# Kernel tuning notes

Measured on AMD Instinct MI355X. Metric: run time of the kernel, lower is better.

The kernel has to match this reference:

```python
import jax, jax.numpy as jnp
import numpy as np

EPS = 1e-6


def layernorm(x, g, b):
    m = jnp.mean(x, axis=-1, keepdims=True)
    v = jnp.var(x, axis=-1, keepdims=True)
    return (x - m) * jax.lax.rsqrt(v + EPS) * g + b


def dwconv(x, w, b):
    # x: (B,H,W,C), w: (kh,kw,1,C) depthwise kernel, SAME padding (stride 1)
    y = jax.lax.conv_general_dilated(
        x, w, window_strides=(1, 1), padding='SAME',
        dimension_numbers=('NHWC', 'HWIO', 'NHWC'),
        feature_group_count=x.shape[-1])
    return y + b


def setup_inputs() -> dict:
    key = jax.random.key(0)
    ks = jax.random.split(key, 16)
    B, H, W, C = 16, 64, 64, 256
    N, F = 8, 1024
    s = 0.02
    return {
        'x': jax.random.normal(ks[0], (B, H, W, C), jnp.float32),
        'mask_h': jax.random.normal(ks[1], (N, H, H), jnp.float32),
        'mask_w': jax.random.normal(ks[2], (N, W, W), jnp.float32),
        'pos_w': jax.random.normal(ks[3], (3, 3, 1, C), jnp.float32) * s,
        'pos_b': jnp.zeros((C,), jnp.float32),
        'ln1_g': jnp.ones((C,), jnp.float32),
        'ln1_b': jnp.zeros((C,), jnp.float32),
        'wq': jax.random.normal(ks[4], (C, C), jnp.float32) * s,
        'bq': jnp.zeros((C,), jnp.float32),
        'wk': jax.random.normal(ks[5], (C, C), jnp.float32) * s,
        'bk': jnp.zeros((C,), jnp.float32),
        'wv': jax.random.normal(ks[6], (C, C), jnp.float32) * s,
        'bv': jnp.zeros((C,), jnp.float32),
        'lepe_w': jax.random.normal(ks[7], (5, 5, 1, C), jnp.float32) * s,
        'lepe_b': jnp.zeros((C,), jnp.float32),
        'wo': jax.random.normal(ks[8], (C, C), jnp.float32) * s,
        'bo': jnp.zeros((C,), jnp.float32),
        'ln2_g': jnp.ones((C,), jnp.float32),
        'ln2_b': jnp.zeros((C,), jnp.float32),
        'fc1_w': jax.random.normal(ks[9], (C, F), jnp.float32) * s,
        'fc1_b': jnp.zeros((F,), jnp.float32),
        'fc2_w': jax.random.normal(ks[10], (F, C), jnp.float32) * s,
        'fc2_b': jnp.zeros((C,), jnp.float32),
    }


NUM_HEADS = 8


def masad(x, mask_h, mask_w, wq, bq, wk, bk, wv, bv, lepe_w, lepe_b, wo, bo):
    # x: (B,H,W,C); decomposed axial retention (MaSAd)
    B, H, W, C = x.shape
    n = NUM_HEADS
    d = C // n
    scaling = d ** (-0.5)
    q = x @ wq + bq
    k = (x @ wk + bk) * scaling
    v = x @ wv + bv
    lepe = dwconv(v, lepe_w, lepe_b)  # (B,H,W,C)
    q5 = q.reshape(B, H, W, n, d)
    k5 = k.reshape(B, H, W, n, d)
    v5 = v.reshape(B, H, W, n, d)
    # --- W-axis attention: scores (B,H,n,W,W)
    qk_w = jnp.einsum('bhqnd,bhknd->bhnqk', q5, k5)
    Aw = jax.nn.softmax(qk_w + mask_w[None, None], axis=-1)
    vo = jnp.einsum('bhnqk,bhknd->bhqnd', Aw, v5)  # (B,H,W,n,d)
    # --- H-axis attention: scores (B,W,n,H,H)
    qk_h = jnp.einsum('bqwnd,bkwnd->bwnqk', q5, k5)
    Ah = jax.nn.softmax(qk_h + mask_h[None, None], axis=-1)
    out = jnp.einsum('bwnqk,bkwnd->bqwnd', Ah, vo)  # (B,H,W,n,d)
    out = out.reshape(B, H, W, C) + lepe
    return out @ wo + bo


def reference(x, mask_h, mask_w, pos_w, pos_b, ln1_g, ln1_b,
              wq, bq, wk, bk, wv, bv, lepe_w, lepe_b, wo, bo,
              ln2_g, ln2_b, fc1_w, fc1_b, fc2_w, fc2_b):
    x = x + dwconv(x, pos_w, pos_b)
    x = x + masad(layernorm(x, ln1_g, ln1_b), mask_h, mask_w,
                  wq, bq, wk, bk, wv, bv, lepe_w, lepe_b, wo, bo)
    h = layernorm(x, ln2_g, ln2_b)
    h = jax.nn.gelu(h @ fc1_w + fc1_b, approximate=False)
    x = x + (h @ fc2_w + fc2_b)
    return x
```

## Files before the change

kernel.cpp:

```cpp
#include <hip/hip_runtime.h>
#include <hip/hip_bf16.h>
#include <math.h>

typedef unsigned short u16;
typedef unsigned int   u32;
typedef float f4   __attribute__((ext_vector_type(4)));
typedef float f32x4 __attribute__((ext_vector_type(4)));
typedef __bf16 bf16x8 __attribute__((ext_vector_type(8)));

#define BDIM 16
#define HDIM 64
#define WDIM 64
#define CDIM 256
#define NHEAD 8
#define DHEAD 32
#define FDIM 1024
#define MROWS (BDIM*HDIM*WDIM)

__device__ inline float blo(u32 u){ return __uint_as_float(u << 16); }
__device__ inline float bhi(u32 u){ return __uint_as_float(u & 0xffff0000u); }

__device__ inline u16 f2bf(float f){
    __bf16 h = (__bf16)f;
    return __builtin_bit_cast(unsigned short, h);
}
__device__ inline __bf16 u2b(u16 x){ return __builtin_bit_cast(__bf16, x); }
__device__ inline u32 pack2(float lo, float hi){
    return (u32)f2bf(lo) | ((u32)f2bf(hi) << 16);
}
__device__ inline void unp8(uint4 u, float* d){
    d[0]=blo(u.x); d[1]=bhi(u.x); d[2]=blo(u.y); d[3]=bhi(u.y);
    d[4]=blo(u.z); d[5]=bhi(u.z); d[6]=blo(u.w); d[7]=bhi(u.w);
}

__global__ __launch_bounds__(256)
void convert_weights_kernel(const float* __restrict__ wq, const float* __restrict__ wk,
                            const float* __restrict__ wv, const float* __restrict__ wo,
                            const float* __restrict__ fc1, const float* __restrict__ fc2,
                            u16* __restrict__ wT)
{
    int i = blockIdx.x * 256 + threadIdx.x;
    const float* src; int K, N, off;
    if (i < 262144) {
        int m = i >> 16;
        src = (m==0) ? wq : (m==1) ? wk : (m==2) ? wv : wo;
        K = 256; N = 256; off = i & 65535;
    } else if (i < 524288) {
        src = fc1; K = 256; N = 1024; off = i - 262144;
    } else {
        src = fc2; K = 1024; N = 256; off = i - 524288;
    }
    int k = off % K, n = off / K;
    wT[i] = f2bf(src[(size_t)k * N + n]);
}

__global__ __launch_bounds__(256)
void posconv_kernel(const float* __restrict__ x, const float* __restrict__ w,
                    const float* __restrict__ bias, float* __restrict__ out)
{
    int idx = blockIdx.x * 256 + threadIdx.x;
    int c = (idx & 63) * 4;
    int p = idx >> 6;
    int wp = p & 63, hp = (p >> 6) & 63, bp = p >> 12;
    f4 acc = *reinterpret_cast<const f4*>(bias + c);
    #pragma unroll
    for (int kh = 0; kh < 3; kh++){
        int hh = hp + kh - 1; if ((unsigned)hh >= 64u) continue;
        #pragma unroll
        for (int kw = 0; kw < 3; kw++){
            int ww = wp + kw - 1; if ((unsigned)ww >= 64u) continue;
            f4 xv = *reinterpret_cast<const f4*>(x + (((size_t)(bp*64 + hh))*64 + ww)*256 + c);
            f4 wv = *reinterpret_cast<const f4*>(w + (size_t)(kh*3 + kw)*256 + c);
            acc += xv * wv;
        }
    }
    f4 ctr = *reinterpret_cast<const f4*>(x + (size_t)p*256 + c);
    *reinterpret_cast<f4*>(out + (size_t)p*256 + c) = ctr + acc;
}

__global__ __launch_bounds__(256)
void lepe_kernel(const u16* __restrict__ v, const float* __restrict__ w,
                 const float* __restrict__ bias, u16* __restrict__ out)
{
    int idx = blockIdx.x * 256 + threadIdx.x;
    int c = (idx & 31) * 8;
    int p = idx >> 5;
    int wp = p & 63, hp = (p >> 6) & 63, bp = p >> 12;
    float acc[8];
    #pragma unroll
    for (int j = 0; j < 8; j++) acc[j] = bias[c + j];
    #pragma unroll
    for (int kh = 0; kh < 5; kh++){
        int hh = hp + kh - 2; if ((unsigned)hh >= 64u) continue;
        #pragma unroll
        for (int kw = 0; kw < 5; kw++){
            int ww = wp + kw - 2; if ((unsigned)ww >= 64u) continue;
            uint4 u = *reinterpret_cast<const uint4*>(v + (((size_t)(bp*64 + hh))*64 + ww)*256 + c);
            float xv[8]; unp8(u, xv);
            const float* wr = w + (size_t)(kh*5 + kw)*256 + c;
            #pragma unroll
            for (int j = 0; j < 8; j++) acc[j] += xv[j] * wr[j];
        }
    }
    uint4 r;
    r.x = pack2(acc[0],acc[1]); r.y = pack2(acc[2],acc[3]);
    r.z = pack2(acc[4],acc[5]); r.w = pack2(acc[6],acc[7]);
    *reinterpret_cast<uint4*>(out + (size_t)p*256 + c) = r;
}

__global__ __launch_bounds__(256)
void ln_kernel(const float* __restrict__ x, const float* __restrict__ g,
               const float* __restrict__ b, u16* __restrict__ y)
{
    int wid = threadIdx.x >> 6, lane = threadIdx.x & 63;
    size_t row = (size_t)blockIdx.x * 4 + wid;
    f4 v = reinterpret_cast<const f4*>(x + row*256)[lane];
    float s  = v.x + v.y + v.z + v.w;
    float q2 = v.x*v.x + v.y*v.y + v.z*v.z + v.w*v.w;
    #pragma unroll
    for (int off = 32; off > 0; off >>= 1){
        s  += __shfl_xor(s,  off);
        q2 += __shfl_xor(q2, off);
    }
    float mean = s * (1.f/256.f);
    float var  = q2 * (1.f/256.f) - mean*mean;
    float rs   = rsqrtf(var + 1e-6f);
    f4 gv = reinterpret_cast<const f4*>(g)[lane];
    f4 bv = reinterpret_cast<const f4*>(b)[lane];
    f4 t = (v - mean) * rs;
    t = t * gv + bv;
    uint2 r;
    r.x = pack2(t.x, t.y); r.y = pack2(t.z, t.w);
    *reinterpret_cast<uint2*>(y + row*256 + (size_t)lane*4) = r;
}

template<int EPI, bool ADD2>
__global__ __launch_bounds__(256)
void gemm_kernel(const u16* __restrict__ A, const u16* __restrict__ A2,
                 const u16* __restrict__ Bt,
                 const float* __restrict__ bias, const float* __restrict__ resid,
                 void* __restrict__ outp, int M, int N, int K, float scale)
{
    __shared__ u16 As[64][32];
    __shared__ u16 Bs[64][32];
    int m0 = blockIdx.x * 64, n0 = blockIdx.y * 64;
    int tid = threadIdx.x, wid = tid >> 6, lane = tid & 63;
    int lr = tid >> 2, lk = (tid & 3) * 8;
    f32x4 acc[4] = {};
    const u16* Ar = A  + (size_t)(m0 + lr) * K + lk;
    const u16* Br = Bt + (size_t)(n0 + lr) * K + lk;
    const u16* A2r = ADD2 ? (A2 + (size_t)(m0 + lr) * K + lk) : nullptr;
    for (int k0 = 0; k0 < K; k0 += 32){
        uint4 ua = *reinterpret_cast<const uint4*>(Ar + k0);
        if constexpr (ADD2){
            uint4 ub = *reinterpret_cast<const uint4*>(A2r + k0);
            float fa[8], fb[8]; unp8(ua, fa); unp8(ub, fb);
            ua.x = pack2(fa[0]+fb[0], fa[1]+fb[1]);
            ua.y = pack2(fa[2]+fb[2], fa[3]+fb[3]);
            ua.z = pack2(fa[4]+fb[4], fa[5]+fb[5]);
            ua.w = pack2(fa[6]+fb[6], fa[7]+fb[7]);
        }
        *reinterpret_cast<uint4*>(&As[lr][lk]) = ua;
        *reinterpret_cast<uint4*>(&Bs[lr][lk]) = *reinterpret_cast<const uint4*>(Br + k0);
        __syncthreads();
        bf16x8 av = *reinterpret_cast<const bf16x8*>(&As[wid*16 + (lane & 15)][(lane >> 4) * 8]);
        #pragma unroll
        for (int nt = 0; nt < 4; nt++){
            bf16x8 bv = *reinterpret_cast<const bf16x8*>(&Bs[nt*16 + (lane & 15)][(lane >> 4) * 8]);
            acc[nt] = __builtin_amdgcn_mfma_f32_16x16x32_bf16(av, bv, acc[nt], 0, 0, 0);
        }
        __syncthreads();
    }
    #pragma unroll
    for (int nt = 0; nt < 4; nt++){
        int col = n0 + nt*16 + (lane & 15);
        float bc = bias[col];
        #pragma unroll
        for (int r = 0; r < 4; r++){
            int row = m0 + wid*16 + ((lane >> 4) << 2) + r;
            float val = acc[nt][r] + bc;
            if constexpr (EPI == 1) val *= scale;
            if constexpr (EPI == 2) val = 0.5f * val * (1.f + erff(val * 0.70710678118654752f));
            if constexpr (EPI == 3){
                size_t o = (size_t)row * N + col;
                reinterpret_cast<float*>(outp)[o] = val + resid[o];
            } else {
                reinterpret_cast<u16*>(outp)[(size_t)row * N + col] = f2bf(val);
            }
        }
    }
}

template<bool HAXIS>
__global__ __launch_bounds__(512, 2)
void attn_mfma_kernel(const u16* __restrict__ q, const u16* __restrict__ k,
                      const u16* __restrict__ v, const float* __restrict__ mask,
                      u16* __restrict__ out)
{
    __shared__ u16 Kl[8][64][40];
    __shared__ u16 Vl[8][64][34];
    __shared__ u16 Pl[8][64][72];
    u16* Ol = &Pl[0][0][0];

    const int tid = threadIdx.x;
    const int lane = tid & 63, wv = tid >> 6;
    const int g = lane >> 4, lm = lane & 15;

    size_t base, RS;
    if constexpr (HAXIS){
        base = (size_t)(blockIdx.x >> 6) * 1048576 + (size_t)(blockIdx.x & 63) * 256;
        RS = 16384;
    } else {
        base = (size_t)blockIdx.x * 16384;
        RS = 256;
    }

    #pragma unroll
    for (int rnd = 0; rnd < 4; rnd++){
        int c = rnd*512 + tid;
        int kk = c >> 5, hd = (c >> 2) & 7, dh = c & 3;
        size_t gco = base + (size_t)kk*RS + hd*32 + dh*8;
        uint4 uk = *reinterpret_cast<const uint4*>(k + gco);
        *reinterpret_cast<uint4*>(&Kl[hd][kk][dh*8]) = uk;
        uint4 uv = *reinterpret_cast<const uint4*>(v + gco);
        *reinterpret_cast<uint4*>(&Vl[hd][kk][dh*8]) = uv;
    }
    bf16x8 qf[4];
    #pragma unroll
    for (int tj = 0; tj < 4; tj++)
        qf[tj] = *reinterpret_cast<const bf16x8*>(q + base + (size_t)(tj*16+lm)*RS + wv*32 + g*8);
    __syncthreads();

    f32x4 st[4][4];
    #pragma unroll
    for (int ti = 0; ti < 4; ti++){
        bf16x8 kf = *reinterpret_cast<const bf16x8*>(&Kl[wv][ti*16+lm][g*8]);
        #pragma unroll
        for (int tj = 0; tj < 4; tj++){
            f32x4 z = {};
            st[ti][tj] = __builtin_amdgcn_mfma_f32_16x16x32_bf16(kf, qf[tj], z, 0, 0, 0);
        }
    }
    #pragma unroll
    for (int tj = 0; tj < 4; tj++){
        const float* mrow = mask + ((size_t)wv*64 + tj*16+lm)*64;
        #pragma unroll
        for (int ti = 0; ti < 4; ti++)
            st[ti][tj] += *reinterpret_cast<const f4*>(mrow + ti*16 + g*4);
    }
    #pragma unroll
    for (int tj = 0; tj < 4; tj++){
        float mx = -1e30f;
        #pragma unroll
        for (int ti = 0; ti < 4; ti++)
            #pragma unroll
            for (int r = 0; r < 4; r++) mx = fmaxf(mx, st[ti][tj][r]);
        mx = fmaxf(mx, __shfl_xor(mx, 16));
        mx = fmaxf(mx, __shfl_xor(mx, 32));
        float sum = 0.f;
        #pragma unroll
        for (int ti = 0; ti < 4; ti++)
            #pragma unroll
            for (int r = 0; r < 4; r++){
                float p = __expf(st[ti][tj][r] - mx);
                st[ti][tj][r] = p; sum += p;
            }
        sum += __shfl_xor(sum, 16);
        sum += __shfl_xor(sum, 32);
        float inv = 1.f / sum;
        #pragma unroll
        for (int ti = 0; ti < 4; ti++){
            uint2 pw;
            pw.x = pack2(st[ti][tj][0]*inv, st[ti][tj][1]*inv);
            pw.y = pack2(st[ti][tj][2]*inv, st[ti][tj][3]*inv);
            *reinterpret_cast<uint2*>(&Pl[wv][tj*16+lm][ti*16+g*4]) = pw;
        }
    }
    f32x4 oc[4][2] = {};
    #pragma unroll
    for (int kb = 0; kb < 2; kb++){
        bf16x8 vf[2];
        #pragma unroll
        for (int dt = 0; dt < 2; dt++)
            #pragma unroll
            for (int j = 0; j < 8; j++)
                vf[dt][j] = u2b(Vl[wv][kb*32 + g*8 + j][dt*16 + lm]);
        #pragma unroll
        for (int ti2 = 0; ti2 < 4; ti2++){
            bf16x8 pf = *reinterpret_cast<const bf16x8*>(&Pl[wv][ti2*16+lm][kb*32 + g*8]);
            oc[ti2][0] = __builtin_amdgcn_mfma_f32_16x16x32_bf16(pf, vf[0], oc[ti2][0], 0, 0, 0);
            oc[ti2][1] = __builtin_amdgcn_mfma_f32_16x16x32_bf16(pf, vf[1], oc[ti2][1], 0, 0, 0);
        }
    }
    __syncthreads();
    #pragma unroll
    for (int ti2 = 0; ti2 < 4; ti2++)
        #pragma unroll
        for (int dt = 0; dt < 2; dt++)
            #pragma unroll
            for (int r = 0; r < 4; r++)
                Ol[((size_t)wv*64 + ti2*16 + g*4 + r)*40 + dt*16 + lm] = f2bf(oc[ti2][dt][r]);
    __syncthreads();
    #pragma unroll
    for (int rnd = 0; rnd < 4; rnd++){
        int c = rnd*512 + tid;
        int row = c >> 5, hd = (c >> 2) & 7, dh = c & 3;
        uint4 u = *reinterpret_cast<const uint4*>(&Ol[((size_t)hd*64 + row)*40 + dh*8]);
        *reinterpret_cast<uint4*>(out + base + (size_t)row*RS + hd*32 + dh*8) = u;
    }
}

extern "C" void kernel_launch(void* const* d_in, const int* in_sizes, int n_in,
                              void* d_out, int out_size, void* d_ws, size_t ws_size,
                              hipStream_t stream)
{
    const float* x      = (const float*)d_in[0];
    const float* mask_h = (const float*)d_in[1];
    const float* mask_w = (const float*)d_in[2];
    const float* pos_w  = (const float*)d_in[3];
    const float* pos_b  = (const float*)d_in[4];
    const float* ln1_g  = (const float*)d_in[5];
    const float* ln1_b  = (const float*)d_in[6];
    const float* wq     = (const float*)d_in[7];
    const float* bq     = (const float*)d_in[8];
    const float* wk     = (const float*)d_in[9];
    const float* bk     = (const float*)d_in[10];
    const float* wv     = (const float*)d_in[11];
    const float* bv     = (const float*)d_in[12];
    const float* lepe_w = (const float*)d_in[13];
    const float* lepe_b = (const float*)d_in[14];
    const float* wo     = (const float*)d_in[15];
    const float* bo     = (const float*)d_in[16];
    const float* ln2_g  = (const float*)d_in[17];
    const float* ln2_b  = (const float*)d_in[18];
    const float* fc1_w  = (const float*)d_in[19];
    const float* fc1_b  = (const float*)d_in[20];
    const float* fc2_w  = (const float*)d_in[21];
    const float* fc2_b  = (const float*)d_in[22];

    const size_t MB = 1u << 20;
    float* x1 = (float*)d_out;

    int Bc = 1;
    for (int c = 16; c >= 1; c >>= 1){
        if (ws_size >= (2 + 10 * (size_t)c) * MB) { Bc = c; break; }
    }

    char* ws = (char*)d_ws;
    u16* wT  = (u16*)ws;
    u16* wqT = wT, *wkT = wT + 65536, *wvT = wT + 131072, *woT = wT + 196608;
    u16* fc1T = wT + 262144, *fc2T = wT + 524288;
    size_t cb = (size_t)Bc * 2 * MB;
    u16* y   = (u16*)(ws + 2*MB);
    u16* qb  = (u16*)(ws + 2*MB + cb);
    u16* kb  = (u16*)(ws + 2*MB + 2*cb);
    u16* vb  = (u16*)(ws + 2*MB + 3*cb);
    u16* lep = (u16*)(ws + 2*MB + 4*cb);
    u16* hb  = qb;

    dim3 blk(256);
    convert_weights_kernel<<<3072, blk, 0, stream>>>(wq, wk, wv, wo, fc1_w, fc2_w, wT);
    posconv_kernel<<<16384, blk, 0, stream>>>(x, pos_w, pos_b, x1);

    const int nchunk = 16 / Bc;
    const int R = Bc * 4096;
    for (int c = 0; c < nchunk; c++){
        float* xc = x1 + (size_t)c * R * 256;
        dim3 gq(R/64, 4), gf(R/64, 16);
        ln_kernel<<<R/4, blk, 0, stream>>>(xc, ln1_g, ln1_b, y);
        gemm_kernel<0,false><<<gq, blk, 0, stream>>>(y, nullptr, wqT, bq, nullptr, qb, R, 256, 256, 1.f);
        gemm_kernel<1,false><<<gq, blk, 0, stream>>>(y, nullptr, wkT, bk, nullptr, kb, R, 256, 256, 0.17677669529663687f);
        gemm_kernel<0,false><<<gq, blk, 0, stream>>>(y, nullptr, wvT, bv, nullptr, vb, R, 256, 256, 1.f);
        lepe_kernel<<<Bc*512, blk, 0, stream>>>(vb, lepe_w, lepe_b, lep);
        attn_mfma_kernel<false><<<Bc*64, 512, 0, stream>>>(qb, kb, vb, mask_w, vb);
        attn_mfma_kernel<true ><<<Bc*64, 512, 0, stream>>>(qb, kb, vb, mask_h, vb);
        gemm_kernel<3,true><<<gq, blk, 0, stream>>>(vb, lep, woT, bo, xc, (void*)xc, R, 256, 256, 1.f);
        ln_kernel<<<R/4, blk, 0, stream>>>(xc, ln2_g, ln2_b, y);
        gemm_kernel<2,false><<<gf, blk, 0, stream>>>(y, nullptr, fc1T, fc1_b, nullptr, hb, R, 1024, 256, 1.f);
        gemm_kernel<3,false><<<gq, blk, 0, stream>>>(hb, nullptr, fc2T, fc2_b, xc, (void*)xc, R, 256, 1024, 1.f);
    }
}
```

Baseline: 725.3 us.

## Replace 64x64 GEMM with 128x128 LDS-direct swizzled tiles and fuse lepe add

Replaces the small 64x64x32 register-staged GEMM with a 128x128x64 tile kernel. It loads global memory straight into LDS with global_load_lds and uses an XOR swizzle to avoid bank conflicts, and each wave computes a 4x4 grid of MFMA tiles. The grid is reordered so N-blocks vary fastest. The lepe residual add moves from the wo GEMM prologue into the H-axis attention epilogue, so the GEMM no longer reads and adds a second operand. The larger tile raises per-block register use and gives fewer blocks per chunk, which may lower occupancy.

```diff
diff --git a/kernel.cpp b/kernel.cpp
--- a/kernel.cpp
+++ b/kernel.cpp
@@ -31,6 +31,11 @@
 __device__ inline void unp8(uint4 u, float* d){
     d[0]=blo(u.x); d[1]=bhi(u.x); d[2]=blo(u.y); d[3]=bhi(u.y);
     d[4]=blo(u.z); d[5]=bhi(u.z); d[6]=blo(u.w); d[7]=bhi(u.w);
+}
+__device__ inline void gld16(const void* g, void* l){
+    __builtin_amdgcn_global_load_lds(
+        (const __attribute__((address_space(1))) void*)g,
+        (__attribute__((address_space(3))) void*)l, 16, 0, 0);
 }
 
 __global__ __launch_bounds__(256)
@@ -134,58 +139,72 @@
     *reinterpret_cast<uint2*>(y + row*256 + (size_t)lane*4) = r;
 }
 
-template<int EPI, bool ADD2>
-__global__ __launch_bounds__(256)
-void gemm_kernel(const u16* __restrict__ A, const u16* __restrict__ A2,
-                 const u16* __restrict__ Bt,
-                 const float* __restrict__ bias, const float* __restrict__ resid,
-                 void* __restrict__ outp, int M, int N, int K, float scale)
-{
-    __shared__ u16 As[64][32];
-    __shared__ u16 Bs[64][32];
-    int m0 = blockIdx.x * 64, n0 = blockIdx.y * 64;
-    int tid = threadIdx.x, wid = tid >> 6, lane = tid & 63;
-    int lr = tid >> 2, lk = (tid & 3) * 8;
-    f32x4 acc[4] = {};
-    const u16* Ar = A  + (size_t)(m0 + lr) * K + lk;
-    const u16* Br = Bt + (size_t)(n0 + lr) * K + lk;
-    const u16* A2r = ADD2 ? (A2 + (size_t)(m0 + lr) * K + lk) : nullptr;
-    for (int k0 = 0; k0 < K; k0 += 32){
-        uint4 ua = *reinterpret_cast<const uint4*>(Ar + k0);
-        if constexpr (ADD2){
-            uint4 ub = *reinterpret_cast<const uint4*>(A2r + k0);
-            float fa[8], fb[8]; unp8(ua, fa); unp8(ub, fb);
-            ua.x = pack2(fa[0]+fb[0], fa[1]+fb[1]);
-            ua.y = pack2(fa[2]+fb[2], fa[3]+fb[3]);
-            ua.z = pack2(fa[4]+fb[4], fa[5]+fb[5]);
-            ua.w = pack2(fa[6]+fb[6], fa[7]+fb[7]);
-        }
-        *reinterpret_cast<uint4*>(&As[lr][lk]) = ua;
-        *reinterpret_cast<uint4*>(&Bs[lr][lk]) = *reinterpret_cast<const uint4*>(Br + k0);
+template<int EPI>
+__global__ __launch_bounds__(256, 2)
+void gemm128_kernel(const u16* __restrict__ A, const u16* __restrict__ Bt,
+                    const float* __restrict__ bias, const float* __restrict__ resid,
+                    void* __restrict__ outp, int M, int N, int K, float scale)
+{
+    __shared__ u16 As[128][64];
+    __shared__ u16 Bs[128][64];
+    const int tid = threadIdx.x;
+    const int wv = tid >> 6, lane = tid & 63;
+    const int g = lane >> 4, lm = lane & 15;
+    const int wr = wv >> 1, wc = wv & 1;
+    const int n0 = blockIdx.x * 128, m0 = blockIdx.y * 128;
+
+    const int srow  = lane >> 3;
+    const int sslot = (lane & 7) ^ srow;
+
+    f32x4 acc[4][4] = {};
+
+    for (int k0 = 0; k0 < K; k0 += 64){
+        #pragma unroll
+        for (int i = 0; i < 4; i++){
+            int rb = wv*32 + i*8;
+            gld16(A  + (size_t)(m0 + rb + srow) * K + k0 + sslot*8, &As[rb][0]);
+            gld16(Bt + (size_t)(n0 + rb + srow) * K + k0 + sslot*8, &Bs[rb][0]);
+        }
         __syncthreads();
-        bf16x8 av = *reinterpret_cast<const bf16x8*>(&As[wid*16 + (lane & 15)][(lane >> 4) * 8]);
-        #pragma unroll
-        for (int nt = 0; nt < 4; nt++){
-            bf16x8 bv = *reinterpret_cast<const bf16x8*>(&Bs[nt*16 + (lane & 15)][(lane >> 4) * 8]);
-            acc[nt] = __builtin_amdgcn_mfma_f32_16x16x32_bf16(av, bv, acc[nt], 0, 0, 0);
+        #pragma unroll
+        for (int ks = 0; ks < 2; ks++){
+            bf16x8 av[4], bv[4];
+            #pragma unroll
+            for (int mt = 0; mt < 4; mt++){
+                int row = wr*64 + mt*16 + lm;
+                av[mt] = *reinterpret_cast<const bf16x8*>(&As[row][((ks*4+g) ^ (row&7))*8]);
+            }
+            #pragma unroll
+            for (int nt = 0; nt < 4; nt++){
+                int col = wc*64 + nt*16 + lm;
+                bv[nt] = *reinterpret_cast<const bf16x8*>(&Bs[col][((ks*4+g) ^ (col&7))*8]);
+            }
+            #pragma unroll
+            for (int mt = 0; mt < 4; mt++)
+                #pragma unroll
+                for (int nt = 0; nt < 4; nt++)
+                    acc[mt][nt] = __builtin_amdgcn_mfma_f32_16x16x32_bf16(av[mt], bv[nt], acc[mt][nt], 0, 0, 0);
         }
         __syncthreads();
     }
     #pragma unroll
     for (int nt = 0; nt < 4; nt++){
-        int col = n0 + nt*16 + (lane & 15);
+        int col = n0 + wc*64 + nt*16 + lm;
         float bc = bias[col];
         #pragma unroll
-        for (int r = 0; r < 4; r++){
-            int row = m0 + wid*16 + ((lane >> 4) << 2) + r;
-            float val = acc[nt][r] + bc;
-            if constexpr (EPI == 1) val *= scale;
-            if constexpr (EPI == 2) val = 0.5f * val * (1.f + erff(val * 0.70710678118654752f));
-            if constexpr (EPI == 3){
-                size_t o = (size_t)row * N + col;
-                reinterpret_cast<float*>(outp)[o] = val + resid[o];
-            } else {
-                reinterpret_cast<u16*>(outp)[(size_t)row * N + col] = f2bf(val);
+        for (int mt = 0; mt < 4; mt++){
+            #pragma unroll
+            for (int r = 0; r < 4; r++){
+                int row = m0 + wr*64 + mt*16 + g*4 + r;
+                float val = acc[mt][nt][r] + bc;
+                if constexpr (EPI == 1) val *= scale;
+                if constexpr (EPI == 2) val = 0.5f * val * (1.f + erff(val * 0.70710678118654752f));
+                if constexpr (EPI == 3){
+                    size_t o = (size_t)row * N + col;
+                    reinterpret_cast<float*>(outp)[o] = val + resid[o];
+                } else {
+                    reinterpret_cast<u16*>(outp)[(size_t)row * N + col] = f2bf(val);
+                }
             }
         }
     }
@@ -195,7 +214,7 @@
 __global__ __launch_bounds__(512, 2)
 void attn_mfma_kernel(const u16* __restrict__ q, const u16* __restrict__ k,
                       const u16* __restrict__ v, const float* __restrict__ mask,
-                      u16* __restrict__ out)
+                      const u16* __restrict__ lep, u16* __restrict__ out)
 {
     __shared__ u16 Kl[8][64][40];
     __shared__ u16 Vl[8][64][34];
@@ -306,7 +325,16 @@
         int c = rnd*512 + tid;
         int row = c >> 5, hd = (c >> 2) & 7, dh = c & 3;
         uint4 u = *reinterpret_cast<const uint4*>(&Ol[((size_t)hd*64 + row)*40 + dh*8]);
-        *reinterpret_cast<uint4*>(out + base + (size_t)row*RS + hd*32 + dh*8) = u;
+        size_t gco = base + (size_t)row*RS + hd*32 + dh*8;
+        if constexpr (HAXIS){
+            uint4 ul = *reinterpret_cast<const uint4*>(lep + gco);
+            float a[8], b2[8]; unp8(u, a); unp8(ul, b2);
+            u.x = pack2(a[0]+b2[0], a[1]+b2[1]);
+            u.y = pack2(a[2]+b2[2], a[3]+b2[3]);
+            u.z = pack2(a[4]+b2[4], a[5]+b2[5]);
+            u.w = pack2(a[6]+b2[6], a[7]+b2[7]);
+        }
+        *reinterpret_cast<uint4*>(out + gco) = u;
     }
 }
 
@@ -366,17 +394,17 @@
     const int R = Bc * 4096;
     for (int c = 0; c < nchunk; c++){
         float* xc = x1 + (size_t)c * R * 256;
-        dim3 gq(R/64, 4), gf(R/64, 16);
+        dim3 gq(2, R/128), gf(8, R/128);
         ln_kernel<<<R/4, blk, 0, stream>>>(xc, ln1_g, ln1_b, y);
-        gemm_kernel<0,false><<<gq, blk, 0, stream>>>(y, nullptr, wqT, bq, nullptr, qb, R, 256, 256, 1.f);
-        gemm_kernel<1,false><<<gq, blk, 0, stream>>>(y, nullptr, wkT, bk, nullptr, kb, R, 256, 256, 0.17677669529663687f);
-        gemm_kernel<0,false><<<gq, blk, 0, stream>>>(y, nullptr, wvT, bv, nullptr, vb, R, 256, 256, 1.f);
+        gemm128_kernel<0><<<gq, blk, 0, stream>>>(y, wqT, bq, nullptr, qb, R, 256, 256, 1.f);
+        gemm128_kernel<1><<<gq, blk, 0, stream>>>(y, wkT, bk, nullptr, kb, R, 256, 256, 0.17677669529663687f);
+        gemm128_kernel<0><<<gq, blk, 0, stream>>>(y, wvT, bv, nullptr, vb, R, 256, 256, 1.f);
         lepe_kernel<<<Bc*512, blk, 0, stream>>>(vb, lepe_w, lepe_b, lep);
-        attn_mfma_kernel<false><<<Bc*64, 512, 0, stream>>>(qb, kb, vb, mask_w, vb);
-        attn_mfma_kernel<true ><<<Bc*64, 512, 0, stream>>>(qb, kb, vb, mask_h, vb);
-        gemm_kernel<3,true><<<gq, blk, 0, stream>>>(vb, lep, woT, bo, xc, (void*)xc, R, 256, 256, 1.f);
+        attn_mfma_kernel<false><<<Bc*64, 512, 0, stream>>>(qb, kb, vb, mask_w, nullptr, vb);
+        attn_mfma_kernel<true ><<<Bc*64, 512, 0, stream>>>(qb, kb, vb, mask_h, lep, vb);
+        gemm128_kernel<3><<<gq, blk, 0, stream>>>(vb, woT, bo, xc, (void*)xc, R, 256, 256, 1.f);
         ln_kernel<<<R/4, blk, 0, stream>>>(xc, ln2_g, ln2_b, y);
-        gemm_kernel<2,false><<<gf, blk, 0, stream>>>(y, nullptr, fc1T, fc1_b, nullptr, hb, R, 1024, 256, 1.f);
-        gemm_kernel<3,false><<<gq, blk, 0, stream>>>(hb, nullptr, fc2T, fc2_b, xc, (void*)xc, R, 256, 1024, 1.f);
-    }
-}
+        gemm128_kernel<2><<<gf, blk, 0, stream>>>(y, fc1T, fc1_b, nullptr, hb, R, 1024, 256, 1.f);
+        gemm128_kernel<3><<<gq, blk, 0, stream>>>(hb, fc2T, fc2_b, xc, (void*)xc, R, 256, 1024, 1.f);
+    }
+}
```

Result: faster. 666.0 us (-8.2%).
